# Performance work log

Hardware: AMD Instinct MI355X
Metric: run time of the kernel (lower is better)

Reference implementation:

```python
import jax, jax.numpy as jnp
import numpy as np
import math

B, S, HID = 2, 2048, 1024
D = 64            # size_per_head
H = HID // D      # num heads = 16
ROT = 32          # rotary_hsize = size_per_head // 2


def _apply_rotary(qk, sinusoids):
    # qk: [B, S, H, D]; sinusoids: [B, 2, S, ROT]
    sin = sinusoids[:, 0, :, None, :]   # [B, S, 1, ROT]
    cos = sinusoids[:, 1, :, None, :]
    qk_rope = qk[..., :ROT]
    # torch.stack([-a[..., ::2], a[..., 1::2]], -1).reshape(a.shape)
    rot2 = jnp.stack([-qk_rope[..., ::2], qk_rope[..., 1::2]], axis=-1).reshape(qk_rope.shape)
    qk_rope = qk_rope * cos + rot2 * sin
    return jnp.concatenate([qk_rope, qk[..., ROT:]], axis=-1)


def setup_inputs() -> dict:
    key = jax.random.key(0)
    ks = jax.random.split(key, 8)
    sc = 1.0 / math.sqrt(HID)
    return {
        "x": jax.random.normal(ks[0], (B, S, HID), jnp.float32),
        "sinusoids": jax.random.normal(ks[1], (B, 2, S, ROT), jnp.float32),
        "attention_bias": jax.random.uniform(ks[2], (B, 1, S, S), jnp.float32),
        "Wq": jax.random.normal(ks[3], (HID, HID), jnp.float32) * sc,
        "bq": jnp.zeros((HID,), jnp.float32),
        "Wk": jax.random.normal(ks[4], (HID, HID), jnp.float32) * sc,
        "bk": jnp.zeros((HID,), jnp.float32),
        "Wv": jax.random.normal(ks[5], (HID, HID), jnp.float32) * sc,
        "bv": jnp.zeros((HID,), jnp.float32),
        "Wo": jax.random.normal(ks[6], (HID, HID), jnp.float32) * sc,
    }


def reference(x, sinusoids, attention_bias, Wq, bq, Wk, bk, Wv, bv, Wo):
    q = (x @ Wq + bq).reshape(B, S, H, D)
    k = (x @ Wk + bk).reshape(B, S, H, D)
    v = (x @ Wv + bv).reshape(B, S, H, D)
    # original concatenates q,k along the heads dim before rotary; since rotary
    # broadcasts over heads, applying it to each separately is identical math
    q = _apply_rotary(q, sinusoids)
    k = _apply_rotary(k, sinusoids)
    q = q / math.sqrt(D)
    scores = jnp.einsum('bqhd,bkhd->bhqk', q, k)          # [B,H,S,S]
    probs = jax.nn.softmax(scores, axis=-1)
    probs = probs * attention_bias                         # multiplicative bias AFTER softmax
    out = jnp.einsum('bhqk,bkhd->bqhd', probs, v)          # [B,S,H,D]
    out = out.reshape(B, S, HID)
    return out @ Wo
```

## Files before the change

### kernel.cpp

```cpp
#include <hip/hip_runtime.h>
#include <math.h>

#define B_   2
#define S_   2048
#define HID_ 1024
#define D_   64
#define H_   16
#define ROT_ 32
#define M_   (B_*S_)

typedef __attribute__((ext_vector_type(4))) short  short4v;
typedef __attribute__((ext_vector_type(8))) short  short8;
typedef __attribute__((ext_vector_type(4))) float  floatx4;
typedef __attribute__((ext_vector_type(16))) float floatx16;
typedef __attribute__((ext_vector_type(2))) unsigned int uint2v;

__device__ __forceinline__ unsigned short f2bf(float f) {
  unsigned int x = __builtin_bit_cast(unsigned int, f);
  x += 0x7fffu + ((x >> 16) & 1u);
  return (unsigned short)(x >> 16);
}
__device__ __forceinline__ unsigned int cvt_pk_bf16(float lo, float hi) {
  unsigned int r;
  asm("v_cvt_pk_bf16_f32 %0, %1, %2" : "=v"(r) : "v"(lo), "v"(hi));
  return r;
}
__device__ __forceinline__ void gload_lds16(const unsigned short* g, unsigned short* l) {
  __builtin_amdgcn_global_load_lds(
      (const __attribute__((address_space(1))) unsigned int*)g,
      (__attribute__((address_space(3))) unsigned int*)l, 16, 0, 0);
}

__global__ void cast_bf16(const float* __restrict__ in, unsigned short* __restrict__ out) {
  int i = (blockIdx.x * 256 + threadIdx.x) * 4;
  floatx4 v = *(const floatx4*)(in + i);
  unsigned short o[4];
  o[0] = f2bf(v[0]); o[1] = f2bf(v[1]); o[2] = f2bf(v[2]); o[3] = f2bf(v[3]);
  *(unsigned long long*)(out + i) = *(unsigned long long*)o;
}

__global__ void transW(const float* __restrict__ W0, const float* __restrict__ W1,
                       const float* __restrict__ W2, const float* __restrict__ W3,
                       unsigned short* __restrict__ T0, unsigned short* __restrict__ T1,
                       unsigned short* __restrict__ T2, unsigned short* __restrict__ T3) {
  const float* W; unsigned short* T;
  int z = blockIdx.z;
  if (z == 0)      { W = W0; T = T0; }
  else if (z == 1) { W = W1; T = T1; }
  else if (z == 2) { W = W2; T = T2; }
  else             { W = W3; T = T3; }
  __shared__ float tile[32][33];
  int bx = blockIdx.x * 32, by = blockIdx.y * 32;
  int tx = threadIdx.x, ty = threadIdx.y;
  #pragma unroll
  for (int j = 0; j < 4; j++)
    tile[ty + j*8][tx] = W[(size_t)(by + ty + j*8) * HID_ + bx + tx];
  __syncthreads();
  #pragma unroll
  for (int j = 0; j < 4; j++)
    T[(size_t)(bx + ty + j*8) * HID_ + by + tx] = f2bf(tile[tx][ty + j*8]);
}

template <int MODE>
__global__ __launch_bounds__(256) void gemm_bt(
    const unsigned short* __restrict__ A,
    const unsigned short* __restrict__ Bt0, const unsigned short* __restrict__ Bt1,
    const unsigned short* __restrict__ Bt2,
    const float* __restrict__ bias0, const float* __restrict__ bias1,
    const float* __restrict__ bias2,
    void* __restrict__ out0, void* __restrict__ out1, void* __restrict__ out2,
    const float* __restrict__ sins, float sc0)
{
  const unsigned short* Bt; const float* bias; void* Out; float sc;
  if (blockIdx.z == 0)      { Bt = Bt0; bias = bias0; Out = out0; sc = sc0; }
  else if (blockIdx.z == 1) { Bt = Bt1; bias = bias1; Out = out1; sc = 1.f; }
  else                      { Bt = Bt2; bias = bias2; Out = out2; sc = 1.f; }
  const int K = HID_, N = HID_;
  int m0 = blockIdx.y * 128, n0 = blockIdx.x * 128;
  __shared__ alignas(16) unsigned short sA[128 * 32];
  __shared__ alignas(16) unsigned short sB[128 * 32];
  int t = threadIdx.x;
  int lane = t & 63, wave = t >> 6;
  int quad = lane >> 4, l16 = lane & 15;
  int wr = wave >> 1, wc = wave & 1;

  int srow = (lane >> 2), scol = (lane & 3) * 8;
  const unsigned short* gA0 = A  + (size_t)(m0 + wave*32 +  0 + srow) * K + scol;
  const unsigned short* gA1 = A  + (size_t)(m0 + wave*32 + 16 + srow) * K + scol;
  const unsigned short* gB0 = Bt + (size_t)(n0 + wave*32 +  0 + srow) * K + scol;
  const unsigned short* gB1 = Bt + (size_t)(n0 + wave*32 + 16 + srow) * K + scol;
  unsigned short* lA0 = sA + (wave*32 +  0) * 32;
  unsigned short* lA1 = sA + (wave*32 + 16) * 32;
  unsigned short* lB0 = sB + (wave*32 +  0) * 32;
  unsigned short* lB1 = sB + (wave*32 + 16) * 32;

  floatx4 acc[4][4];
  #pragma unroll
  for (int i = 0; i < 4; i++)
    #pragma unroll
    for (int j = 0; j < 4; j++)
      acc[i][j] = (floatx4){0.f, 0.f, 0.f, 0.f};

  for (int k0 = 0; k0 < K; k0 += 32) {
    gload_lds16(gA0 + k0, lA0);
    gload_lds16(gA1 + k0, lA1);
    gload_lds16(gB0 + k0, lB0);
    gload_lds16(gB1 + k0, lB1);
    __syncthreads();
    short8 af[4], bf[4];
    #pragma unroll
    for (int i = 0; i < 4; i++) {
      af[i] = *(const short8*)(sA + (wr * 64 + i * 16 + l16) * 32 + quad * 8);
      bf[i] = *(const short8*)(sB + (wc * 64 + i * 16 + l16) * 32 + quad * 8);
    }
    #pragma unroll
    for (int i = 0; i < 4; i++)
      #pragma unroll
      for (int j = 0; j < 4; j++)
        acc[i][j] = __builtin_amdgcn_mfma_f32_16x16x32_bf16(af[i], bf[j], acc[i][j], 0, 0, 0);
    __syncthreads();
  }

  #pragma unroll
  for (int i = 0; i < 4; i++) {
    int mbase = m0 + wr * 64 + i * 16 + quad * 4;
    #pragma unroll
    for (int j = 0; j < 4; j++) {
      int n = n0 + wc * 64 + j * 16 + l16;
      float bv = bias ? bias[n] : 0.f;
      if (MODE == 1) {
        #pragma unroll
        for (int r = 0; r < 4; r++)
          ((float*)Out)[(size_t)(mbase + r) * N + n] = acc[i][j][r] + bv;
      } else if (blockIdx.z == 2) {
        int bb = mbase >> 11, ss = mbase & 2047;
        int hh = n >> 6, dd = n & 63;
        unsigned short pk[4];
        #pragma unroll
        for (int r = 0; r < 4; r++) pk[r] = f2bf(acc[i][j][r] + bv);
        *(unsigned long long*)((unsigned short*)Out +
            (((size_t)(bb * H_ + hh) * D_ + dd) * S_ + ss)) = *(unsigned long long*)pk;
      } else if (j < 2) {
        int jh = j * 16 + l16;
        #pragma unroll
        for (int r = 0; r < 4; r++) {
          int row = mbase + r, bb = row >> 11, ss = row & 2047;
          float sn = sins[((size_t)(bb * 2 + 0) * S_ + ss) * ROT_ + jh];
          float cs = sins[((size_t)(bb * 2 + 1) * S_ + ss) * ROT_ + jh];
          float f = (jh & 1) ? (cs + sn) : (cs - sn);
          ((unsigned short*)Out)[(size_t)row * N + n] = f2bf((acc[i][j][r] + bv) * f * sc);
        }
      } else {
        #pragma unroll
        for (int r = 0; r < 4; r++)
          ((unsigned short*)Out)[(size_t)(mbase + r) * N + n] = f2bf((acc[i][j][r] + bv) * sc);
      }
    }
  }
}

__global__ __launch_bounds__(256) void gemm_bt64(
    const unsigned short* __restrict__ A, const unsigned short* __restrict__ Bt,
    float* __restrict__ Out)
{
  const int K = HID_, N = HID_;
  int m0 = blockIdx.y * 128, n0 = blockIdx.x * 64;
  __shared__ alignas(16) unsigned short sA[128 * 32];
  __shared__ alignas(16) unsigned short sB[64 * 32];
  int t = threadIdx.x;
  int lane = t & 63, wave = t >> 6;
  int quad = lane >> 4, l16 = lane & 15;
  int wr = wave >> 1, wc = wave & 1;

  int srow = lane >> 2, scol = (lane & 3) * 8;
  const unsigned short* gA0 = A  + (size_t)(m0 + wave*32 +  0 + srow) * K + scol;
  const unsigned short* gA1 = A  + (size_t)(m0 + wave*32 + 16 + srow) * K + scol;
  const unsigned short* gB0 = Bt + (size_t)(n0 + wave*16 + srow) * K + scol;
  unsigned short* lA0 = sA + (wave*32 +  0) * 32;
  unsigned short* lA1 = sA + (wave*32 + 16) * 32;
  unsigned short* lB0 = sB + (wave*16) * 32;

  floatx4 acc[4][2];
  #pragma unroll
  for (int i = 0; i < 4; i++)
    #pragma unroll
    for (int j = 0; j < 2; j++)
      acc[i][j] = (floatx4){0.f, 0.f, 0.f, 0.f};

  for (int k0 = 0; k0 < K; k0 += 32) {
    gload_lds16(gA0 + k0, lA0);
    gload_lds16(gA1 + k0, lA1);
    gload_lds16(gB0 + k0, lB0);
    __syncthreads();
    short8 af[4], bf[2];
    #pragma unroll
    for (int i = 0; i < 4; i++)
      af[i] = *(const short8*)(sA + (wr * 64 + i * 16 + l16) * 32 + quad * 8);
    #pragma unroll
    for (int j = 0; j < 2; j++)
      bf[j] = *(const short8*)(sB + (wc * 32 + j * 16 + l16) * 32 + quad * 8);
    #pragma unroll
    for (int i = 0; i < 4; i++)
      #pragma unroll
      for (int j = 0; j < 2; j++)
        acc[i][j] = __builtin_amdgcn_mfma_f32_16x16x32_bf16(af[i], bf[j], acc[i][j], 0, 0, 0);
    __syncthreads();
  }

  #pragma unroll
  for (int i = 0; i < 4; i++) {
    int mbase = m0 + wr * 64 + i * 16 + quad * 4;
    #pragma unroll
    for (int j = 0; j < 2; j++) {
      int n = n0 + wc * 32 + j * 16 + l16;
      #pragma unroll
      for (int r = 0; r < 4; r++)
        Out[(size_t)(mbase + r) * N + n] = acc[i][j][r];
    }
  }
}

__global__ __launch_bounds__(512, 1) void attn(
    const unsigned short* __restrict__ Q, const unsigned short* __restrict__ Kb,
    const unsigned short* __restrict__ Vt, const float* __restrict__ bias,
    unsigned short* __restrict__ Out)
{
  int b = blockIdx.z, h = blockIdx.y;
  int t = threadIdx.x;
  int lane = t & 63, wave = t >> 6;
  int g = wave >> 2, wg = wave & 3;
  int l32 = lane & 31, hl = lane >> 5;
  int s7 = l32 & 7;
  int q0 = blockIdx.x * 128 + wg * 32;
  const int RS = H_ * D_;
  const int NT = S_ / 128;

  __shared__ alignas(16) unsigned short smem[65536];
  unsigned short* bg = smem + g * 32768;

  const unsigned short* Qbase = Q + ((size_t)(b * S_) * H_ + h) * D_;
  const unsigned short* Kbase = Kb + ((size_t)(b * S_) * H_ + h) * D_;
  const unsigned short* Vbase = Vt + ((size_t)(b * H_) + h) * D_ * S_;

  short8 qf[4];
  {
    const unsigned short* qp = Qbase + (size_t)(q0 + l32) * RS + 8 * hl;
    qf[0] = *(const short8*)(qp);
    qf[1] = *(const short8*)(qp + 16);
    qf[2] = *(const short8*)(qp + 32);
    qf[3] = *(const short8*)(qp + 48);
  }

  int tg = t & 255;
  int row0 = tg >> 3;
  int csw  = (tg & 7) ^ (row0 & 7);
  const unsigned short* gK0 = Kbase + (size_t)(g*1024 + row0)      * RS + csw * 8;
  const unsigned short* gK1 = Kbase + (size_t)(g*1024 + row0 + 32) * RS + csw * 8;
  const unsigned short* gV0 = Vbase + (size_t)(row0)      * S_ + g*1024 + csw * 8;
  const unsigned short* gV1 = Vbase + (size_t)(row0 + 32) * S_ + g*1024 + csw * 8;

  const float* bp = bias + (size_t)b * S_ * S_ + (size_t)(q0 + l32) * S_ + g * 1024 + 4 * hl;

#define STAGE(bi, tk) do { \
    unsigned short* kb_ = bg + (bi) * 4096; \
    unsigned short* vb_ = bg + 16384 + (bi) * 4096; \
    size_t ko_ = (size_t)(tk) * 64 * RS; int vo_ = (tk) * 64; \
    gload_lds16(gK0 + ko_, kb_ + tg * 8); \
    gload_lds16(gK1 + ko_, kb_ + (256 + tg) * 8); \
    gload_lds16(gV0 + vo_, vb_ + tg * 8); \
    gload_lds16(gV1 + vo_, vb_ + (256 + tg) * 8); \
  } while (0)

  float l_run = 0.f;
  floatx16 o0, o1;
  #pragma unroll
  for (int r = 0; r < 16; r++) { o0[r] = 0.f; o1[r] = 0.f; }

  STAGE(0, 0);
  floatx4 b0[4], b1[4];
  #pragma unroll
  for (int rg = 0; rg < 4; rg++) {
    b0[rg] = *(const floatx4*)(bp + 8 * rg);
    b1[rg] = *(const floatx4*)(bp + 32 + 8 * rg);
  }
  STAGE(1, 1);
  STAGE(2, 2);

  for (int it = 0; it < NT; ++it) {
    int cur = it & 3;
    asm volatile("s_waitcnt vmcnt(16)" ::: "memory");
    __builtin_amdgcn_s_barrier();
    __builtin_amdgcn_sched_barrier(0);
    if (it < NT - 3) STAGE((it + 3) & 3, it + 3);

    const unsigned short* kbuf = bg + cur * 4096;
    const unsigned short* vbuf = bg + 16384 + cur * 4096;
    int itn = ((it + 1) & (NT - 1)) * 64;

    floatx16 st;
    #pragma unroll
    for (int r = 0; r < 16; r++) st[r] = 0.f;
    __builtin_amdgcn_s_setprio(1);
    #pragma unroll
    for (int ks = 0; ks < 4; ks++) {
      short8 kf = *(const short8*)(kbuf + l32 * 64 + (((2 * ks + hl) ^ s7) * 8));
      st = __builtin_amdgcn_mfma_f32_32x32x16_bf16(kf, qf[ks], st, 0, 0, 0);
    }
    __builtin_amdgcn_s_setprio(0);

    short4v pf0[4];
    #pragma unroll
    for (int rg = 0; rg < 4; rg++) {
      float p0 = __builtin_amdgcn_exp2f(st[rg * 4 + 0]);
      float p1 = __builtin_amdgcn_exp2f(st[rg * 4 + 1]);
      float p2 = __builtin_amdgcn_exp2f(st[rg * 4 + 2]);
      float p3 = __builtin_amdgcn_exp2f(st[rg * 4 + 3]);
      l_run += (p0 + p1) + (p2 + p3);
      uint2v u;
      u[0] = cvt_pk_bf16(p0 * b0[rg][0], p1 * b0[rg][1]);
      u[1] = cvt_pk_bf16(p2 * b0[rg][2], p3 * b0[rg][3]);
      pf0[rg] = __builtin_bit_cast(short4v, u);
    }
    #pragma unroll
    for (int rg = 0; rg < 4; rg++)
      b0[rg] = *(const floatx4*)(bp + itn + 8 * rg);

    floatx16 st1;
    #pragma unroll
    for (int r = 0; r < 16; r++) st1[r] = 0.f;
    __builtin_amdgcn_s_setprio(1);
    #pragma unroll
    for (int ks = 0; ks < 4; ks++) {
      short8 kf = *(const short8*)(kbuf + (32 + l32) * 64 + (((2 * ks + hl) ^ s7) * 8));
      st1 = __builtin_amdgcn_mfma_f32_32x32x16_bf16(kf, qf[ks], st1, 0, 0, 0);
    }
    #pragma unroll
    for (int gg = 0; gg < 4; gg++) {
      int ch = (gg ^ s7) * 8 + hl * 4;
      short4v vf0 = *(const short4v*)(vbuf + l32 * 64 + ch);
      short4v vf1 = *(const short4v*)(vbuf + (32 + l32) * 64 + ch);
      o0 = __builtin_amdgcn_mfma_f32_32x32x8bf16_1k(pf0[gg], vf0, o0, 0, 0, 0);
      o1 = __builtin_amdgcn_mfma_f32_32x32x8bf16_1k(pf0[gg], vf1, o1, 0, 0, 0);
    }
    __builtin_amdgcn_s_setprio(0);

    short4v pf1[4];
    #pragma unroll
    for (int rg = 0; rg < 4; rg++) {
      float p0 = __builtin_amdgcn_exp2f(st1[rg * 4 + 0]);
      float p1 = __builtin_amdgcn_exp2f(st1[rg * 4 + 1]);
      float p2 = __builtin_amdgcn_exp2f(st1[rg * 4 + 2]);
      float p3 = __builtin_amdgcn_exp2f(st1[rg * 4 + 3]);
      l_run += (p0 + p1) + (p2 + p3);
      uint2v u;
      u[0] = cvt_pk_bf16(p0 * b1[rg][0], p1 * b1[rg][1]);
      u[1] = cvt_pk_bf16(p2 * b1[rg][2], p3 * b1[rg][3]);
      pf1[rg] = __builtin_bit_cast(short4v, u);
    }
    #pragma unroll
    for (int rg = 0; rg < 4; rg++)
      b1[rg] = *(const floatx4*)(bp + itn + 32 + 8 * rg);

    __builtin_amdgcn_s_setprio(1);
    #pragma unroll
    for (int gg = 0; gg < 4; gg++) {
      int ch = ((4 + gg) ^ s7) * 8 + hl * 4;
      short4v vf0 = *(const short4v*)(vbuf + l32 * 64 + ch);
      short4v vf1 = *(const short4v*)(vbuf + (32 + l32) * 64 + ch);
      o0 = __builtin_amdgcn_mfma_f32_32x32x8bf16_1k(pf1[gg], vf0, o0, 0, 0, 0);
      o1 = __builtin_amdgcn_mfma_f32_32x32x8bf16_1k(pf1[gg], vf1, o1, 0, 0, 0);
    }
    __builtin_amdgcn_s_setprio(0);
  }
#undef STAGE

  float l2 = l_run + __shfl_xor(l_run, 32);

  float* sO = (float*)smem;
  float* sL = (float*)(smem + 16384);

  __syncthreads();
  if (g == 1) {
    #pragma unroll
    for (int r = 0; r < 16; r++) {
      int ql = (r & 3) + 8 * (r >> 2) + 4 * hl;
      sO[(wg * 32 + ql) * 64 + l32]      = o0[r];
      sO[(wg * 32 + ql) * 64 + 32 + l32] = o1[r];
    }
    if (hl == 0) sL[wg * 32 + l32] = l2;
  }
  __syncthreads();
  if (g == 0) {
    float linv = __builtin_amdgcn_rcpf(l2 + sL[wg * 32 + l32]);
    #pragma unroll
    for (int r = 0; r < 16; r++) {
      int ql = (r & 3) + 8 * (r >> 2) + 4 * hl;
      float sc = __shfl(linv, ql);
      size_t base = ((size_t)(b * S_ + q0 + ql) * H_ + h) * D_;
      float a0 = o0[r] + sO[(wg * 32 + ql) * 64 + l32];
      float a1 = o1[r] + sO[(wg * 32 + ql) * 64 + 32 + l32];
      Out[base + l32]      = f2bf(a0 * sc);
      Out[base + 32 + l32] = f2bf(a1 * sc);
    }
  }
}

extern "C" void kernel_launch(void* const* d_in, const int* in_sizes, int n_in,
                              void* d_out, int out_size, void* d_ws, size_t ws_size,
                              hipStream_t stream) {
  (void)in_sizes; (void)n_in; (void)out_size; (void)ws_size;
  const float* x    = (const float*)d_in[0];
  const float* sins = (const float*)d_in[1];
  const float* ab   = (const float*)d_in[2];
  const float* Wq   = (const float*)d_in[3];
  const float* bq   = (const float*)d_in[4];
  const float* Wk   = (const float*)d_in[5];
  const float* bk   = (const float*)d_in[6];
  const float* Wv   = (const float*)d_in[7];
  const float* bv   = (const float*)d_in[8];
  const float* Wo   = (const float*)d_in[9];
  float* out = (float*)d_out;
  char* ws = (char*)d_ws;

  unsigned short* xb  = (unsigned short*)(ws);
  unsigned short* Wqt = (unsigned short*)(ws + ((size_t) 8 << 20));
  unsigned short* Wkt = (unsigned short*)(ws + ((size_t)10 << 20));
  unsigned short* Wvt = (unsigned short*)(ws + ((size_t)12 << 20));
  unsigned short* Wot = (unsigned short*)(ws + ((size_t)14 << 20));
  unsigned short* Qb  = (unsigned short*)(ws + ((size_t)16 << 20));
  unsigned short* Kb  = (unsigned short*)(ws + ((size_t)24 << 20));
  unsigned short* Vtb = (unsigned short*)(ws + ((size_t)32 << 20));
  unsigned short* Ab  = (unsigned short*)(ws + ((size_t)40 << 20));

  const float c1 = 0.125f * 1.44269504088896f;

  cast_bf16<<<dim3((M_ * HID_) / (256 * 4)), dim3(256), 0, stream>>>(x, xb);
  transW<<<dim3(32, 32, 4), dim3(32, 8), 0, stream>>>(Wq, Wk, Wv, Wo, Wqt, Wkt, Wvt, Wot);
  gemm_bt<0><<<dim3(8, 32, 3), dim3(256), 0, stream>>>(xb, Wqt, Wkt, Wvt, bq, bk, bv,
                                                       Qb, Kb, Vtb, sins, c1);
  attn<<<dim3(S_ / 128, H_, B_), dim3(512), 0, stream>>>(Qb, Kb, Vtb, ab, Ab);
  gemm_bt64<<<dim3(HID_ / 64, M_ / 128), dim3(256), 0, stream>>>(Ab, Wot, out);
}
```

Measured before the change: 274.2 us.

## Use 32x32x16 MFMA for PV via cross-lane shuffle of probability fragments

Replaces the eight 32x32x8 PV MFMAs per half-tile with four 32x32x16 MFMAs. To match the larger K-operand layout, the packed bf16 probabilities are exchanged between half-waves with __shfl_xor. V is now read from LDS with 8-element loads. The bias prefetch for the next tile moves to the top of the iteration into separate registers, and the loop is unrolled by two. The aim is to halve the MFMA instruction count and LDS read count for PV, at the cost of extra shuffles and higher register pressure.

```diff
diff --git a/kernel.cpp b/kernel.cpp
--- a/kernel.cpp
+++ b/kernel.cpp
@@ -13,7 +13,7 @@
 typedef __attribute__((ext_vector_type(8))) short  short8;
 typedef __attribute__((ext_vector_type(4))) float  floatx4;
 typedef __attribute__((ext_vector_type(16))) float floatx16;
-typedef __attribute__((ext_vector_type(2))) unsigned int uint2v;
+typedef __attribute__((ext_vector_type(4))) unsigned int uint4v;
 
 __device__ __forceinline__ unsigned short f2bf(float f) {
   unsigned int x = __builtin_bit_cast(unsigned int, f);
@@ -277,7 +277,7 @@
   for (int r = 0; r < 16; r++) { o0[r] = 0.f; o1[r] = 0.f; }
 
   STAGE(0, 0);
-  floatx4 b0[4], b1[4];
+  floatx4 b0[4], b1[4], bn0[4], bn1[4];
   #pragma unroll
   for (int rg = 0; rg < 4; rg++) {
     b0[rg] = *(const floatx4*)(bp + 8 * rg);
@@ -286,91 +286,72 @@
   STAGE(1, 1);
   STAGE(2, 2);
 
+  #pragma unroll 2
   for (int it = 0; it < NT; ++it) {
     int cur = it & 3;
     asm volatile("s_waitcnt vmcnt(16)" ::: "memory");
     __builtin_amdgcn_s_barrier();
+
+    int itn = ((it + 1) & (NT - 1)) * 64;
+    #pragma unroll
+    for (int rg = 0; rg < 4; rg++) {
+      bn0[rg] = *(const floatx4*)(bp + itn + 8 * rg);
+      bn1[rg] = *(const floatx4*)(bp + itn + 32 + 8 * rg);
+    }
     __builtin_amdgcn_sched_barrier(0);
     if (it < NT - 3) STAGE((it + 3) & 3, it + 3);
 
     const unsigned short* kbuf = bg + cur * 4096;
     const unsigned short* vbuf = bg + 16384 + cur * 4096;
-    int itn = ((it + 1) & (NT - 1)) * 64;
-
-    floatx16 st;
-    #pragma unroll
-    for (int r = 0; r < 16; r++) st[r] = 0.f;
-    __builtin_amdgcn_s_setprio(1);
-    #pragma unroll
-    for (int ks = 0; ks < 4; ks++) {
-      short8 kf = *(const short8*)(kbuf + l32 * 64 + (((2 * ks + hl) ^ s7) * 8));
-      st = __builtin_amdgcn_mfma_f32_32x32x16_bf16(kf, qf[ks], st, 0, 0, 0);
-    }
-    __builtin_amdgcn_s_setprio(0);
-
-    short4v pf0[4];
-    #pragma unroll
-    for (int rg = 0; rg < 4; rg++) {
-      float p0 = __builtin_amdgcn_exp2f(st[rg * 4 + 0]);
-      float p1 = __builtin_amdgcn_exp2f(st[rg * 4 + 1]);
-      float p2 = __builtin_amdgcn_exp2f(st[rg * 4 + 2]);
-      float p3 = __builtin_amdgcn_exp2f(st[rg * 4 + 3]);
-      l_run += (p0 + p1) + (p2 + p3);
-      uint2v u;
-      u[0] = cvt_pk_bf16(p0 * b0[rg][0], p1 * b0[rg][1]);
-      u[1] = cvt_pk_bf16(p2 * b0[rg][2], p3 * b0[rg][3]);
-      pf0[rg] = __builtin_bit_cast(short4v, u);
-    }
-    #pragma unroll
-    for (int rg = 0; rg < 4; rg++)
-      b0[rg] = *(const floatx4*)(bp + itn + 8 * rg);
-
-    floatx16 st1;
-    #pragma unroll
-    for (int r = 0; r < 16; r++) st1[r] = 0.f;
-    __builtin_amdgcn_s_setprio(1);
-    #pragma unroll
-    for (int ks = 0; ks < 4; ks++) {
-      short8 kf = *(const short8*)(kbuf + (32 + l32) * 64 + (((2 * ks + hl) ^ s7) * 8));
-      st1 = __builtin_amdgcn_mfma_f32_32x32x16_bf16(kf, qf[ks], st1, 0, 0, 0);
-    }
-    #pragma unroll
-    for (int gg = 0; gg < 4; gg++) {
-      int ch = (gg ^ s7) * 8 + hl * 4;
-      short4v vf0 = *(const short4v*)(vbuf + l32 * 64 + ch);
-      short4v vf1 = *(const short4v*)(vbuf + (32 + l32) * 64 + ch);
-      o0 = __builtin_amdgcn_mfma_f32_32x32x8bf16_1k(pf0[gg], vf0, o0, 0, 0, 0);
-      o1 = __builtin_amdgcn_mfma_f32_32x32x8bf16_1k(pf0[gg], vf1, o1, 0, 0, 0);
-    }
-    __builtin_amdgcn_s_setprio(0);
-
-    short4v pf1[4];
-    #pragma unroll
-    for (int rg = 0; rg < 4; rg++) {
-      float p0 = __builtin_amdgcn_exp2f(st1[rg * 4 + 0]);
-      float p1 = __builtin_amdgcn_exp2f(st1[rg * 4 + 1]);
-      float p2 = __builtin_amdgcn_exp2f(st1[rg * 4 + 2]);
-      float p3 = __builtin_amdgcn_exp2f(st1[rg * 4 + 3]);
-      l_run += (p0 + p1) + (p2 + p3);
-      uint2v u;
-      u[0] = cvt_pk_bf16(p0 * b1[rg][0], p1 * b1[rg][1]);
-      u[1] = cvt_pk_bf16(p2 * b1[rg][2], p3 * b1[rg][3]);
-      pf1[rg] = __builtin_bit_cast(short4v, u);
-    }
-    #pragma unroll
-    for (int rg = 0; rg < 4; rg++)
-      b1[rg] = *(const floatx4*)(bp + itn + 32 + 8 * rg);
-
-    __builtin_amdgcn_s_setprio(1);
-    #pragma unroll
-    for (int gg = 0; gg < 4; gg++) {
-      int ch = ((4 + gg) ^ s7) * 8 + hl * 4;
-      short4v vf0 = *(const short4v*)(vbuf + l32 * 64 + ch);
-      short4v vf1 = *(const short4v*)(vbuf + (32 + l32) * 64 + ch);
-      o0 = __builtin_amdgcn_mfma_f32_32x32x8bf16_1k(pf1[gg], vf0, o0, 0, 0, 0);
-      o1 = __builtin_amdgcn_mfma_f32_32x32x8bf16_1k(pf1[gg], vf1, o1, 0, 0, 0);
-    }
-    __builtin_amdgcn_s_setprio(0);
+
+    #pragma unroll
+    for (int cc = 0; cc < 2; cc++) {
+      floatx16 st;
+      #pragma unroll
+      for (int r = 0; r < 16; r++) st[r] = 0.f;
+      __builtin_amdgcn_s_setprio(1);
+      #pragma unroll
+      for (int ks = 0; ks < 4; ks++) {
+        short8 kf = *(const short8*)(kbuf + (cc * 32 + l32) * 64 + (((2 * ks + hl) ^ s7) * 8));
+        st = __builtin_amdgcn_mfma_f32_32x32x16_bf16(kf, qf[ks], st, 0, 0, 0);
+      }
+      __builtin_amdgcn_s_setprio(0);
+
+      const floatx4* bl = cc ? b1 : b0;
+      unsigned int pk[8], sw[8];
+      #pragma unroll
+      for (int m = 0; m < 4; m++) {
+        float p0 = __builtin_amdgcn_exp2f(st[m * 4 + 0]);
+        float p1 = __builtin_amdgcn_exp2f(st[m * 4 + 1]);
+        float p2 = __builtin_amdgcn_exp2f(st[m * 4 + 2]);
+        float p3 = __builtin_amdgcn_exp2f(st[m * 4 + 3]);
+        l_run += (p0 + p1) + (p2 + p3);
+        pk[m * 2 + 0] = cvt_pk_bf16(p0 * bl[m][0], p1 * bl[m][1]);
+        pk[m * 2 + 1] = cvt_pk_bf16(p2 * bl[m][2], p3 * bl[m][3]);
+      }
+      #pragma unroll
+      for (int u = 0; u < 8; u++) sw[u] = __shfl_xor(pk[u], 32);
+
+      __builtin_amdgcn_s_setprio(1);
+      #pragma unroll
+      for (int kk = 0; kk < 2; kk++) {
+        uint4v w;
+        w[0] = hl ? sw[4 * kk + 2] : pk[4 * kk + 0];
+        w[1] = hl ? sw[4 * kk + 3] : pk[4 * kk + 1];
+        w[2] = hl ? pk[4 * kk + 2] : sw[4 * kk + 0];
+        w[3] = hl ? pk[4 * kk + 3] : sw[4 * kk + 1];
+        short8 af = __builtin_bit_cast(short8, w);
+        int ch = ((4 * cc + 2 * kk + hl) ^ s7) * 8;
+        short8 vf0 = *(const short8*)(vbuf + (l32)      * 64 + ch);
+        short8 vf1 = *(const short8*)(vbuf + (32 + l32) * 64 + ch);
+        o0 = __builtin_amdgcn_mfma_f32_32x32x16_bf16(af, vf0, o0, 0, 0, 0);
+        o1 = __builtin_amdgcn_mfma_f32_32x32x16_bf16(af, vf1, o1, 0, 0, 0);
+      }
+      __builtin_amdgcn_s_setprio(0);
+    }
+
+    #pragma unroll
+    for (int rg = 0; rg < 4; rg++) { b0[rg] = bn0[rg]; b1[rg] = bn1[rg]; }
   }
 #undef STAGE
 
```

Result: slower. 298.2 us (+8.8%).
